# Kernel optimization log

Hardware: AMD Instinct MI355X
Metric: run time of the kernel (lower is better)

## Reference

```python
import jax, jax.numpy as jnp
import numpy as np

N = 12000      # total nodes
T = 6000       # tail (query) nodes
H = 4000       # head (key/value) nodes
D = 256        # att_hidd_dim
NUM_HEADS = 8
HEAD_DIM = D // NUM_HEADS
EDGE_VOCAB = 64


def setup_inputs() -> dict:
    key = jax.random.key(0)
    ks = jax.random.split(key, 16)
    inp = {
        "query": jax.random.normal(ks[0], (N, D), jnp.float32),
        "key": jax.random.normal(ks[1], (N, D), jnp.float32),
        "value": jax.random.normal(ks[2], (N, D), jnp.float32),
        "adj_matrix": jax.random.randint(ks[3], (T, H), 0, 2, jnp.int32),
        "c_indices": jax.random.randint(ks[4], (T, H), 0, EDGE_VOCAB, jnp.int32),
        "ground_ind_tail": jnp.arange(T, dtype=jnp.int32),
        "ground_ind_head": jnp.arange(H, dtype=jnp.int32) + T,  # disjoint bipartite sets
        "Wq": 0.02 * jax.random.normal(ks[5], (D, D), jnp.float32),
        "bq": jnp.zeros((D,), jnp.float32),
        "Wk": 0.02 * jax.random.normal(ks[6], (D, D), jnp.float32),
        "bk": jnp.zeros((D,), jnp.float32),
        "Wv": 0.02 * jax.random.normal(ks[7], (D, D), jnp.float32),
        "bv": jnp.zeros((D,), jnp.float32),
        "Wo": 0.02 * jax.random.normal(ks[8], (D, D), jnp.float32),
        "bo": jnp.zeros((D,), jnp.float32),
        "edge_emb": 0.02 * jax.random.normal(ks[9], (EDGE_VOCAB, NUM_HEADS), jnp.float32),
    }
    return inp


def reference(query, key, value, adj_matrix, c_indices, ground_ind_tail,
              ground_ind_head, Wq, bq, Wk, bk, Wv, bv, Wo, bo, edge_emb):
    scaling = HEAD_DIM ** -0.5
    # gather + project; [heads, T, hd] / [heads, H, hd]
    q_tail = ((query[ground_ind_tail] @ Wq.T + bq) * scaling).reshape(T, NUM_HEADS, HEAD_DIM).swapaxes(0, 1)
    k_head = (key[ground_ind_head] @ Wk.T + bk).reshape(H, NUM_HEADS, HEAD_DIM).swapaxes(0, 1)
    v_head = (value[ground_ind_head] @ Wv.T + bv).reshape(H, NUM_HEADS, HEAD_DIM).swapaxes(0, 1)

    tail_mask = jnp.where(adj_matrix == 0, -1e9, 0.0)[None]              # [1, T, H]
    edge_bias = edge_emb[c_indices].transpose(2, 0, 1)                    # [heads, T, H]

    scores = jnp.einsum('htd,hsd->hts', q_tail, k_head) + tail_mask + edge_bias
    attn = jax.nn.softmax(scores, axis=-1)
    out_tail = jnp.einsum('hts,hsd->htd', attn, v_head)                   # [heads, T, hd]

    attn_all = jnp.zeros((NUM_HEADS, N, HEAD_DIM), query.dtype)
    attn_all = attn_all.at[:, ground_ind_tail].set(out_tail)
    attn_all = attn_all.at[:, ground_ind_head].set(
        query[ground_ind_head].reshape(H, NUM_HEADS, HEAD_DIM).swapaxes(0, 1))
    attn_all = attn_all.swapaxes(0, 1).reshape(N, D)                      # [N, D]
    return attn_all @ Wo.T + bo
```

## Files before the change

### kernel.cpp

```cpp
#include <hip/hip_runtime.h>
#include <hip/hip_bf16.h>

#define T_N 6000
#define H_N 4000
#define N_N 12000
#define DIM 256
#define NHEAD 8
#define HDIM 32
#define SCALING 0.17677669529663687f
#define LOG2E 1.4426950408889634f
#define NTT 375
#define NST 125

typedef __attribute__((ext_vector_type(8))) short bf16x8;
typedef __attribute__((ext_vector_type(4))) float f32x4;

union BF8U { bf16x8 v; unsigned int w[4]; __hip_bfloat16 h[8]; };

static __device__ __forceinline__ unsigned int cvt_pk_bf16(float a, float b) {
  unsigned int r;
  asm("v_cvt_pk_bf16_f32 %0, %1, %2" : "=v"(r) : "v"(a), "v"(b));
  return r;
}

static __device__ __forceinline__ void proj_body(
    int role, const float* __restrict__ X, const int* __restrict__ idx,
    const float* __restrict__ W, const float* __restrict__ bvec,
    __hip_bfloat16* __restrict__ outf, int rows, float scale, int bx,
    char* As, char* Bs)
{
  const int tid = threadIdx.x;
  const int w = tid >> 6;
  const int lane = tid & 63;
  const int q = lane >> 4;
  const int t = lane & 15;
  const int n0 = (bx & 7) * 32;
  const int m0 = (bx >> 3) * 64;

  for (int i = tid; i < 2048; i += 256) {
    const int row = i >> 5, c16 = i & 31;
    BF8U u;
    u.w[0] = 0; u.w[1] = 0; u.w[2] = 0; u.w[3] = 0;
    const int gr = m0 + row;
    if (gr < rows) {
      const int src = idx ? idx[gr] : gr;
      const float* sp = X + (size_t)src * DIM + c16 * 8;
      const float4 x0 = *reinterpret_cast<const float4*>(sp);
      const float4 x1 = *reinterpret_cast<const float4*>(sp + 4);
      u.w[0] = cvt_pk_bf16(x0.x, x0.y);
      u.w[1] = cvt_pk_bf16(x0.z, x0.w);
      u.w[2] = cvt_pk_bf16(x1.x, x1.y);
      u.w[3] = cvt_pk_bf16(x1.z, x1.w);
    }
    *reinterpret_cast<bf16x8*>(As + ((row * 512 + c16 * 16) ^ ((row & 7) << 4))) = u.v;
  }
  for (int i = tid; i < 1024; i += 256) {
    const int row = i >> 5, c16 = i & 31;
    const float* sp = W + (size_t)(n0 + row) * DIM + c16 * 8;
    const float4 x0 = *reinterpret_cast<const float4*>(sp);
    const float4 x1 = *reinterpret_cast<const float4*>(sp + 4);
    BF8U u;
    u.w[0] = cvt_pk_bf16(x0.x, x0.y);
    u.w[1] = cvt_pk_bf16(x0.z, x0.w);
    u.w[2] = cvt_pk_bf16(x1.x, x1.y);
    u.w[3] = cvt_pk_bf16(x1.z, x1.w);
    *reinterpret_cast<bf16x8*>(Bs + ((row * 512 + c16 * 16) ^ ((row & 7) << 4))) = u.v;
  }
  __syncthreads();

  f32x4 acc0 = {0.f, 0.f, 0.f, 0.f};
  f32x4 acc1 = {0.f, 0.f, 0.f, 0.f};
#pragma unroll
  for (int kk = 0; kk < 8; kk++) {
    const int arow = w * 16 + t;
    const bf16x8 af = *reinterpret_cast<const bf16x8*>(
        As + ((arow * 512 + (kk * 32 + q * 8) * 2) ^ ((arow & 7) << 4)));
    const bf16x8 bf0 = *reinterpret_cast<const bf16x8*>(
        Bs + ((t * 512 + (kk * 32 + q * 8) * 2) ^ ((t & 7) << 4)));
    const bf16x8 bf1 = *reinterpret_cast<const bf16x8*>(
        Bs + (((16 + t) * 512 + (kk * 32 + q * 8) * 2) ^ (((16 + t) & 7) << 4)));
    acc0 = __builtin_amdgcn_mfma_f32_16x16x32_bf16(af, bf0, acc0, 0, 0, 0);
    acc1 = __builtin_amdgcn_mfma_f32_16x16x32_bf16(af, bf1, acc1, 0, 0, 0);
  }

#pragma unroll
  for (int r = 0; r < 4; r++) {
    const int grow = m0 + w * 16 + q * 4 + r;
    if (grow >= rows) continue;
    const float a0 = acc0[r], a1 = acc1[r];
    const int jj[2] = {n0 + t, n0 + 16 + t};
    const float vv[2] = {(a0 + bvec[jj[0]]) * scale, (a1 + bvec[jj[1]]) * scale};
#pragma unroll
    for (int f = 0; f < 2; f++) {
      const int j = jj[f];
      const __hip_bfloat16 hv = __float2bfloat16(vv[f]);
      const int h = j >> 5;
      size_t idxo;
      if (role == 1) {
        idxo = (((size_t)h * NTT + (grow >> 4)) * 64 + ((j & 31) >> 3) * 16 +
                (grow & 15)) * 8 + (j & 7);
      } else if (role == 2) {
        idxo = (((size_t)h * 250 + (grow >> 4)) * 64 + ((j & 31) >> 3) * 16 +
                (grow & 15)) * 8 + (j & 7);
      } else {
        const int dh = (j & 31) >> 4, dl = j & 15;
        const int sl = grow & 31;
        const int qv = (sl & 15) >> 2;
        const int ev = (sl & 3) | (((sl >> 4) & 1) << 2);
        idxo = ((((size_t)h * 2 + dh) * NST + (grow >> 5)) * 64 +
                qv * 16 + dl) * 8 + ev;
      }
      outf[idxo] = hv;
    }
  }
}

#define NBQ 752
#define NBK 504
#define NBV 504
#define NBC 1000
#define NBP 23438

__global__ __launch_bounds__(256) void fused_pre(
    const float* __restrict__ query, const float* __restrict__ key,
    const float* __restrict__ value, const int* __restrict__ adj,
    const int* __restrict__ cind, const int* __restrict__ tail_idx,
    const int* __restrict__ head_idx,
    const float* __restrict__ Wq, const float* __restrict__ bq,
    const float* __restrict__ Wk, const float* __restrict__ bk,
    const float* __restrict__ Wv, const float* __restrict__ bv,
    __hip_bfloat16* __restrict__ Qf, __hip_bfloat16* __restrict__ Kf,
    __hip_bfloat16* __restrict__ Vf, unsigned int* __restrict__ pc,
    __hip_bfloat16* __restrict__ Ab)
{
  __shared__ __align__(16) char As[64 * 512];
  __shared__ __align__(16) char Bs[32 * 512];

  const int bx = blockIdx.x;
  if (bx < NBQ) {
    proj_body(1, query, tail_idx, Wq, bq, Qf, T_N, SCALING * LOG2E, bx, As, Bs);
  } else if (bx < NBQ + NBK) {
    proj_body(2, key, head_idx, Wk, bk, Kf, H_N, 1.f, bx - NBQ, As, Bs);
  } else if (bx < NBQ + NBK + NBV) {
    proj_body(3, value, head_idx, Wv, bv, Vf, H_N, 1.f, bx - NBQ - NBK, As, Bs);
  } else if (bx < NBQ + NBK + NBV + NBC) {
    const int b = bx - NBQ - NBK - NBV;
    const int rr = b * 4 + (threadIdx.x >> 6);
    const int lane = threadIdx.x & 63;
    const int row = head_idx[rr];
    const float4 v = *reinterpret_cast<const float4*>(
        query + (size_t)row * DIM + lane * 4);
    uint2 o;
    o.x = cvt_pk_bf16(v.x, v.y);
    o.y = cvt_pk_bf16(v.z, v.w);
    *reinterpret_cast<uint2*>(Ab + (size_t)row * DIM + lane * 4) = o;
  } else {
    const int i = (bx - NBQ - NBK - NBV - NBC) * 256 + threadIdx.x;
    if (i >= NTT * NST * 128) return;
    const int tl = i & 15;
    const int gi = (i >> 4) & 7;
    const int rem = i >> 7;
    const int st = rem % NST;
    const int tt = rem / NST;
    const int t = tt * 16 + tl;
    const int s0 = st * 32 + gi * 4;
    const int4 c4 = *reinterpret_cast<const int4*>(cind + (size_t)t * H_N + s0);
    const int4 a4 = *reinterpret_cast<const int4*>(adj + (size_t)t * H_N + s0);
    unsigned int w = 0;
    w |= (unsigned)(((c4.x & 63) << 2) | (a4.x ? 1 : 0));
    w |= (unsigned)(((c4.y & 63) << 2) | (a4.y ? 1 : 0)) << 8;
    w |= (unsigned)(((c4.z & 63) << 2) | (a4.z ? 1 : 0)) << 16;
    w |= (unsigned)(((c4.w & 63) << 2) | (a4.w ? 1 : 0)) << 24;
    pc[i] = w;
  }
}

__global__ __launch_bounds__(256, 8) void attn_mfma(
    const __hip_bfloat16* __restrict__ Qf, const __hip_bfloat16* __restrict__ Kf,
    const __hip_bfloat16* __restrict__ Vf, const unsigned int* __restrict__ pc,
    const float* __restrict__ edge_emb, const int* __restrict__ tail_idx,
    __hip_bfloat16* __restrict__ Ab)
{
  __shared__ float mg[3][64][10];

  const int tid = threadIdx.x;
  const int cs = tid >> 6;
  const int lane = tid & 63;
  const int q = lane >> 4;
  const int t = lane & 15;
  const int h = blockIdx.y;
  const int tt = blockIdx.x;
  const int hbase = h * HDIM;

  const int etab = __float_as_int(edge_emb[lane * NHEAD + h] * LOG2E);

  const bf16x8 qf = *reinterpret_cast<const bf16x8*>(
      Qf + (((size_t)h * NTT + tt) * 64 + lane) * 8);

  const int stBeg = (cs * NST) >> 2;
  const int stEnd = ((cs + 1) * NST) >> 2;

  const unsigned int* pcp = pc + (size_t)(tt * NST + stBeg) * 128 + q * 16 + t;
  const __hip_bfloat16* kp = Kf + (((size_t)h * 250 + stBeg * 2) * 64 + lane) * 8;
  const __hip_bfloat16* vp = Vf + (((size_t)h * 2 * NST + stBeg) * 64 + lane) * 8;
  const size_t VD = (size_t)NST * 64 * 8;

  f32x4 oacc0 = {0.f, 0.f, 0.f, 0.f};
  f32x4 oacc1 = {0.f, 0.f, 0.f, 0.f};
  float Lacc = 0.f;

  unsigned int npc0 = pcp[0], npc1 = pcp[64];
  bf16x8 nk0 = *reinterpret_cast<const bf16x8*>(kp);
  bf16x8 nk1 = *reinterpret_cast<const bf16x8*>(kp + 512);
  bf16x8 nv0 = *reinterpret_cast<const bf16x8*>(vp);
  bf16x8 nv1 = *reinterpret_cast<const bf16x8*>(vp + VD);

  for (int st = stBeg; st < stEnd; ++st) {
    const unsigned int cpc0 = npc0, cpc1 = npc1;
    const bf16x8 kf0 = nk0, kf1 = nk1, vf0 = nv0, vf1 = nv1;

    const f32x4 z = {0.f, 0.f, 0.f, 0.f};
    const f32x4 s_lo = __builtin_amdgcn_mfma_f32_16x16x32_bf16(kf0, qf, z, 0, 0, 0);
    const f32x4 s_hi = __builtin_amdgcn_mfma_f32_16x16x32_bf16(kf1, qf, z, 0, 0, 0);

    if (st + 1 < stEnd) {
      pcp += 128; kp += 1024; vp += 512;
      npc0 = pcp[0];
      npc1 = pcp[64];
      nk0 = *reinterpret_cast<const bf16x8*>(kp);
      nk1 = *reinterpret_cast<const bf16x8*>(kp + 512);
      nv0 = *reinterpret_cast<const bf16x8*>(vp);
      nv1 = *reinterpret_cast<const bf16x8*>(vp + VD);
    }

    float p[8];
#pragma unroll
    for (int r = 0; r < 4; r++) {
      const unsigned b0 = (cpc0 >> (r * 8)) & 0xffu;
      const unsigned b1 = (cpc1 >> (r * 8)) & 0xffu;
      const int e0 = __builtin_amdgcn_ds_bpermute((int)(b0 & 0xfcu), etab);
      const int e1 = __builtin_amdgcn_ds_bpermute((int)(b1 & 0xfcu), etab);
      const float bb0 = (b0 & 1u) ? __int_as_float(e0) : -1e9f;
      const float bb1 = (b1 & 1u) ? __int_as_float(e1) : -1e9f;
      p[r] = __builtin_amdgcn_exp2f(s_lo[r] + bb0);
      p[r + 4] = __builtin_amdgcn_exp2f(s_hi[r] + bb1);
    }
#pragma unroll
    for (int r = 0; r < 8; r++) Lacc += p[r];

    BF8U pu;
    pu.w[0] = cvt_pk_bf16(p[0], p[1]);
    pu.w[1] = cvt_pk_bf16(p[2], p[3]);
    pu.w[2] = cvt_pk_bf16(p[4], p[5]);
    pu.w[3] = cvt_pk_bf16(p[6], p[7]);

    oacc0 = __builtin_amdgcn_mfma_f32_16x16x32_bf16(vf0, pu.v, oacc0, 0, 0, 0);
    oacc1 = __builtin_amdgcn_mfma_f32_16x16x32_bf16(vf1, pu.v, oacc1, 0, 0, 0);
  }

  Lacc += __shfl_xor(Lacc, 16, 64);
  Lacc += __shfl_xor(Lacc, 32, 64);

  if (cs) {
#pragma unroll
    for (int r = 0; r < 4; r++) {
      mg[cs - 1][lane][r] = oacc0[r];
      mg[cs - 1][lane][4 + r] = oacc1[r];
    }
    mg[cs - 1][lane][8] = Lacc;
  }
  __syncthreads();
  if (!cs) {
    float L = Lacc;
    float o[8];
#pragma unroll
    for (int r = 0; r < 8; r++) o[r] = (r < 4) ? oacc0[r] : oacc1[r - 4];
#pragma unroll
    for (int c = 0; c < 3; c++) {
      L += mg[c][lane][8];
#pragma unroll
      for (int r = 0; r < 8; r++) o[r] += mg[c][lane][r];
    }
    const float inv = 1.f / L;
    const int row = tail_idx[tt * 16 + t];
    __hip_bfloat16* dst = Ab + (size_t)row * DIM + hbase + q * 4;
    uint2 w0, w1;
    w0.x = cvt_pk_bf16(o[0] * inv, o[1] * inv);
    w0.y = cvt_pk_bf16(o[2] * inv, o[3] * inv);
    w1.x = cvt_pk_bf16(o[4] * inv, o[5] * inv);
    w1.y = cvt_pk_bf16(o[6] * inv, o[7] * inv);
    *reinterpret_cast<uint2*>(dst) = w0;
    *reinterpret_cast<uint2*>(dst + 16) = w1;
  }
}

__global__ __launch_bounds__(256) void oproj_mfma(
    const __hip_bfloat16* __restrict__ Ab, const float* __restrict__ Wo,
    const float* __restrict__ bo, float* __restrict__ out)
{
  __shared__ __align__(16) char As[64 * 512];
  __shared__ __align__(16) char Bs[32 * 512];

  const int tid = threadIdx.x;
  const int w = tid >> 6;
  const int lane = tid & 63;
  const int bl = lane & 15;
  const int q = lane >> 4;
  const int n0 = blockIdx.x * 32;
  const int m0 = blockIdx.y * 64;

  for (int i = tid; i < 2048; i += 256) {
    const int row = i >> 5, c16 = i & 31;
    bf16x8 v = {0, 0, 0, 0, 0, 0, 0, 0};
    const int gr = m0 + row;
    if (gr < N_N)
      v = *reinterpret_cast<const bf16x8*>(Ab + (size_t)gr * DIM + c16 * 8);
    *reinterpret_cast<bf16x8*>(As + ((row * 512 + c16 * 16) ^ ((row & 7) << 4))) = v;
  }
  for (int i = tid; i < 1024; i += 256) {
    const int row = i >> 5, c16 = i & 31;
    const float* src = Wo + (size_t)(n0 + row) * DIM + c16 * 8;
    const float4 x0 = *reinterpret_cast<const float4*>(src);
    const float4 x1 = *reinterpret_cast<const float4*>(src + 4);
    BF8U u;
    u.w[0] = cvt_pk_bf16(x0.x, x0.y);
    u.w[1] = cvt_pk_bf16(x0.z, x0.w);
    u.w[2] = cvt_pk_bf16(x1.x, x1.y);
    u.w[3] = cvt_pk_bf16(x1.z, x1.w);
    *reinterpret_cast<bf16x8*>(Bs + ((row * 512 + c16 * 16) ^ ((row & 7) << 4))) = u.v;
  }
  __syncthreads();

  f32x4 acc0 = {0.f, 0.f, 0.f, 0.f};
  f32x4 acc1 = {0.f, 0.f, 0.f, 0.f};
#pragma unroll
  for (int kk = 0; kk < 8; kk++) {
    const int arow = w * 16 + bl;
    const bf16x8 af = *reinterpret_cast<const bf16x8*>(
        As + ((arow * 512 + (kk * 32 + q * 8) * 2) ^ ((arow & 7) << 4)));
    const bf16x8 bf0 = *reinterpret_cast<const bf16x8*>(
        Bs + ((bl * 512 + (kk * 32 + q * 8) * 2) ^ ((bl & 7) << 4)));
    const int brow = 16 + bl;
    const bf16x8 bf1 = *reinterpret_cast<const bf16x8*>(
        Bs + ((brow * 512 + (kk * 32 + q * 8) * 2) ^ ((brow & 7) << 4)));
    acc0 = __builtin_amdgcn_mfma_f32_16x16x32_bf16(af, bf0, acc0, 0, 0, 0);
    acc1 = __builtin_amdgcn_mfma_f32_16x16x32_bf16(af, bf1, acc1, 0, 0, 0);
  }

#pragma unroll
  for (int r = 0; r < 4; r++) {
    const int grow = m0 + w * 16 + q * 4 + r;
    if (grow < N_N) {
      const int j0 = n0 + bl;
      const int j1 = n0 + 16 + bl;
      out[(size_t)grow * DIM + j0] = acc0[r] + bo[j0];
      out[(size_t)grow * DIM + j1] = acc1[r] + bo[j1];
    }
  }
}

extern "C" void kernel_launch(void* const* d_in, const int* in_sizes, int n_in,
                              void* d_out, int out_size, void* d_ws, size_t ws_size,
                              hipStream_t stream)
{
  const float* query    = (const float*)d_in[0];
  const float* key      = (const float*)d_in[1];
  const float* value    = (const float*)d_in[2];
  const int*   adj      = (const int*)d_in[3];
  const int*   cind     = (const int*)d_in[4];
  const int*   tail_idx = (const int*)d_in[5];
  const int*   head_idx = (const int*)d_in[6];
  const float* Wq = (const float*)d_in[7];
  const float* bq = (const float*)d_in[8];
  const float* Wk = (const float*)d_in[9];
  const float* bk = (const float*)d_in[10];
  const float* Wv = (const float*)d_in[11];
  const float* bv = (const float*)d_in[12];
  const float* Wo = (const float*)d_in[13];
  const float* bo = (const float*)d_in[14];
  const float* edge_emb = (const float*)d_in[15];

  float* out = (float*)d_out;
  char*  ws  = (char*)d_ws;

  __hip_bfloat16* Ab = (__hip_bfloat16*)ws;
  __hip_bfloat16* Qf = (__hip_bfloat16*)(ws + 6144000);
  __hip_bfloat16* Kf = (__hip_bfloat16*)(ws + 9216000);
  __hip_bfloat16* Vf = (__hip_bfloat16*)(ws + 11264000);
  unsigned int*   pc = (unsigned int*)(ws + 13312000);

  hipMemsetAsync(Ab, 0, (size_t)N_N * DIM * sizeof(__hip_bfloat16), stream);

  fused_pre<<<dim3(NBQ + NBK + NBV + NBC + NBP), dim3(256), 0, stream>>>(
      query, key, value, adj, cind, tail_idx, head_idx,
      Wq, bq, Wk, bk, Wv, bv, Qf, Kf, Vf, pc, Ab);

  attn_mfma<<<dim3(NTT, NHEAD), dim3(256), 0, stream>>>(
      Qf, Kf, Vf, pc, edge_emb, tail_idx, Ab);

  oproj_mfma<<<dim3(8, (N_N + 63) / 64), dim3(256), 0, stream>>>(
      Ab, Wo, bo, out);
}
```

Baseline: 168.2 us.

## Split mask packing into grid-stride kernel and prefetch edge bias one step ahead

The adjacency/edge-index packing moves out of the fused preprocessing kernel into its own grid-stride kernel with 2048 blocks, replacing roughly 23k single-shot blocks. The projection kernel keeps only the Q/K/V projections and the head-row copy. In the attention loop, the bpermute edge-bias lookups for the next tile now run after the PV MFMAs, so the LDS permute latency overlaps the MFMA work instead of sitting between the score MFMA and the exp. This adds a kernel launch and holds eight extra live bias registers, which could affect occupancy.

```diff
diff --git a/kernel.cpp b/kernel.cpp
--- a/kernel.cpp
+++ b/kernel.cpp
@@ -11,6 +11,7 @@
 #define LOG2E 1.4426950408889634f
 #define NTT 375
 #define NST 125
+#define PCW (NTT * NST * 128)
 
 typedef __attribute__((ext_vector_type(8))) short bf16x8;
 typedef __attribute__((ext_vector_type(4))) float f32x4;
@@ -21,6 +22,30 @@
   unsigned int r;
   asm("v_cvt_pk_bf16_f32 %0, %1, %2" : "=v"(r) : "v"(a), "v"(b));
   return r;
+}
+
+__global__ __launch_bounds__(256) void pack_pc(
+    const int* __restrict__ adj, const int* __restrict__ cind,
+    unsigned int* __restrict__ pc)
+{
+  const int stride = gridDim.x * 256;
+  for (int i = blockIdx.x * 256 + threadIdx.x; i < PCW; i += stride) {
+    const int tl = i & 15;
+    const int gi = (i >> 4) & 7;
+    const int rem = i >> 7;
+    const int st = rem % NST;
+    const int tt = rem / NST;
+    const int t = tt * 16 + tl;
+    const int s0 = st * 32 + gi * 4;
+    const int4 c4 = *reinterpret_cast<const int4*>(cind + (size_t)t * H_N + s0);
+    const int4 a4 = *reinterpret_cast<const int4*>(adj + (size_t)t * H_N + s0);
+    unsigned int w = 0;
+    w |= (unsigned)(((c4.x & 63) << 2) | (a4.x ? 1 : 0));
+    w |= (unsigned)(((c4.y & 63) << 2) | (a4.y ? 1 : 0)) << 8;
+    w |= (unsigned)(((c4.z & 63) << 2) | (a4.z ? 1 : 0)) << 16;
+    w |= (unsigned)(((c4.w & 63) << 2) | (a4.w ? 1 : 0)) << 24;
+    pc[i] = w;
+  }
 }
 
 static __device__ __forceinline__ void proj_body(
@@ -119,19 +144,16 @@
 #define NBK 504
 #define NBV 504
 #define NBC 1000
-#define NBP 23438
-
-__global__ __launch_bounds__(256) void fused_pre(
+
+__global__ __launch_bounds__(256) void proj_all(
     const float* __restrict__ query, const float* __restrict__ key,
-    const float* __restrict__ value, const int* __restrict__ adj,
-    const int* __restrict__ cind, const int* __restrict__ tail_idx,
+    const float* __restrict__ value, const int* __restrict__ tail_idx,
     const int* __restrict__ head_idx,
     const float* __restrict__ Wq, const float* __restrict__ bq,
     const float* __restrict__ Wk, const float* __restrict__ bk,
     const float* __restrict__ Wv, const float* __restrict__ bv,
     __hip_bfloat16* __restrict__ Qf, __hip_bfloat16* __restrict__ Kf,
-    __hip_bfloat16* __restrict__ Vf, unsigned int* __restrict__ pc,
-    __hip_bfloat16* __restrict__ Ab)
+    __hip_bfloat16* __restrict__ Vf, __hip_bfloat16* __restrict__ Ab)
 {
   __shared__ __align__(16) char As[64 * 512];
   __shared__ __align__(16) char Bs[32 * 512];
@@ -143,7 +165,7 @@
     proj_body(2, key, head_idx, Wk, bk, Kf, H_N, 1.f, bx - NBQ, As, Bs);
   } else if (bx < NBQ + NBK + NBV) {
     proj_body(3, value, head_idx, Wv, bv, Vf, H_N, 1.f, bx - NBQ - NBK, As, Bs);
-  } else if (bx < NBQ + NBK + NBV + NBC) {
+  } else {
     const int b = bx - NBQ - NBK - NBV;
     const int rr = b * 4 + (threadIdx.x >> 6);
     const int lane = threadIdx.x & 63;
@@ -154,24 +176,6 @@
     o.x = cvt_pk_bf16(v.x, v.y);
     o.y = cvt_pk_bf16(v.z, v.w);
     *reinterpret_cast<uint2*>(Ab + (size_t)row * DIM + lane * 4) = o;
-  } else {
-    const int i = (bx - NBQ - NBK - NBV - NBC) * 256 + threadIdx.x;
-    if (i >= NTT * NST * 128) return;
-    const int tl = i & 15;
-    const int gi = (i >> 4) & 7;
-    const int rem = i >> 7;
-    const int st = rem % NST;
-    const int tt = rem / NST;
-    const int t = tt * 16 + tl;
-    const int s0 = st * 32 + gi * 4;
-    const int4 c4 = *reinterpret_cast<const int4*>(cind + (size_t)t * H_N + s0);
-    const int4 a4 = *reinterpret_cast<const int4*>(adj + (size_t)t * H_N + s0);
-    unsigned int w = 0;
-    w |= (unsigned)(((c4.x & 63) << 2) | (a4.x ? 1 : 0));
-    w |= (unsigned)(((c4.y & 63) << 2) | (a4.y ? 1 : 0)) << 8;
-    w |= (unsigned)(((c4.z & 63) << 2) | (a4.z ? 1 : 0)) << 16;
-    w |= (unsigned)(((c4.w & 63) << 2) | (a4.w ? 1 : 0)) << 24;
-    pc[i] = w;
   }
 }
 
@@ -215,18 +219,33 @@
   bf16x8 nv0 = *reinterpret_cast<const bf16x8*>(vp);
   bf16x8 nv1 = *reinterpret_cast<const bf16x8*>(vp + VD);
 
+  float bb[8];
+#pragma unroll
+  for (int r = 0; r < 4; r++) {
+    const unsigned b0 = (npc0 >> (r * 8)) & 0xffu;
+    const unsigned b1 = (npc1 >> (r * 8)) & 0xffu;
+    const int e0 = __builtin_amdgcn_ds_bpermute((int)(b0 & 0xfcu), etab);
+    const int e1 = __builtin_amdgcn_ds_bpermute((int)(b1 & 0xfcu), etab);
+    bb[r] = (b0 & 1u) ? __int_as_float(e0) : -1e9f;
+    bb[r + 4] = (b1 & 1u) ? __int_as_float(e1) : -1e9f;
+  }
+
   for (int st = stBeg; st < stEnd; ++st) {
-    const unsigned int cpc0 = npc0, cpc1 = npc1;
     const bf16x8 kf0 = nk0, kf1 = nk1, vf0 = nv0, vf1 = nv1;
+    const bool more = (st + 1 < stEnd);
+
+    if (more) {
+      pcp += 128;
+      npc0 = pcp[0];
+      npc1 = pcp[64];
+    }
 
     const f32x4 z = {0.f, 0.f, 0.f, 0.f};
     const f32x4 s_lo = __builtin_amdgcn_mfma_f32_16x16x32_bf16(kf0, qf, z, 0, 0, 0);
     const f32x4 s_hi = __builtin_amdgcn_mfma_f32_16x16x32_bf16(kf1, qf, z, 0, 0, 0);
 
-    if (st + 1 < stEnd) {
-      pcp += 128; kp += 1024; vp += 512;
-      npc0 = pcp[0];
-      npc1 = pcp[64];
+    if (more) {
+      kp += 1024; vp += 512;
       nk0 = *reinterpret_cast<const bf16x8*>(kp);
       nk1 = *reinterpret_cast<const bf16x8*>(kp + 512);
       nv0 = *reinterpret_cast<const bf16x8*>(vp);
@@ -235,18 +254,10 @@
 
     float p[8];
 #pragma unroll
-    for (int r = 0; r < 4; r++) {
-      const unsigned b0 = (cpc0 >> (r * 8)) & 0xffu;
-      const unsigned b1 = (cpc1 >> (r * 8)) & 0xffu;
-      const int e0 = __builtin_amdgcn_ds_bpermute((int)(b0 & 0xfcu), etab);
-      const int e1 = __builtin_amdgcn_ds_bpermute((int)(b1 & 0xfcu), etab);
-      const float bb0 = (b0 & 1u) ? __int_as_float(e0) : -1e9f;
-      const float bb1 = (b1 & 1u) ? __int_as_float(e1) : -1e9f;
-      p[r] = __builtin_amdgcn_exp2f(s_lo[r] + bb0);
-      p[r + 4] = __builtin_amdgcn_exp2f(s_hi[r] + bb1);
-    }
-#pragma unroll
-    for (int r = 0; r < 8; r++) Lacc += p[r];
+    for (int r = 0; r < 8; r++) {
+      p[r] = __builtin_amdgcn_exp2f(((r < 4) ? s_lo[r] : s_hi[r - 4]) + bb[r]);
+      Lacc += p[r];
+    }
 
     BF8U pu;
     pu.w[0] = cvt_pk_bf16(p[0], p[1]);
@@ -256,6 +267,18 @@
 
     oacc0 = __builtin_amdgcn_mfma_f32_16x16x32_bf16(vf0, pu.v, oacc0, 0, 0, 0);
     oacc1 = __builtin_amdgcn_mfma_f32_16x16x32_bf16(vf1, pu.v, oacc1, 0, 0, 0);
+
+    if (more) {
+#pragma unroll
+      for (int r = 0; r < 4; r++) {
+        const unsigned b0 = (npc0 >> (r * 8)) & 0xffu;
+        const unsigned b1 = (npc1 >> (r * 8)) & 0xffu;
+        const int e0 = __builtin_amdgcn_ds_bpermute((int)(b0 & 0xfcu), etab);
+        const int e1 = __builtin_amdgcn_ds_bpermute((int)(b1 & 0xfcu), etab);
+        bb[r] = (b0 & 1u) ? __int_as_float(e0) : -1e9f;
+        bb[r + 4] = (b1 & 1u) ? __int_as_float(e1) : -1e9f;
+      }
+    }
   }
 
   Lacc += __shfl_xor(Lacc, 16, 64);
@@ -391,9 +414,11 @@
 
   hipMemsetAsync(Ab, 0, (size_t)N_N * DIM * sizeof(__hip_bfloat16), stream);
 
-  fused_pre<<<dim3(NBQ + NBK + NBV + NBC + NBP), dim3(256), 0, stream>>>(
-      query, key, value, adj, cind, tail_idx, head_idx,
-      Wq, bq, Wk, bk, Wv, bv, Qf, Kf, Vf, pc, Ab);
+  pack_pc<<<dim3(2048), dim3(256), 0, stream>>>(adj, cind, pc);
+
+  proj_all<<<dim3(NBQ + NBK + NBV + NBC), dim3(256), 0, stream>>>(
+      query, key, value, tail_idx, head_idx,
+      Wq, bq, Wk, bk, Wv, bv, Qf, Kf, Vf, Ab);
 
   attn_mfma<<<dim3(NTT, NHEAD), dim3(256), 0, stream>>>(
       Qf, Kf, Vf, pc, edge_emb, tail_idx, Ab);
```

New measurement: 329.2 us. 1.96x slower.
